# Kernel tuning notes

Measured on AMD Instinct MI355X. Metric: run time of the kernel, lower is better.

Reference implementation:

```python
import jax, jax.numpy as jnp
import numpy as np

NY, NX = 1024, 2048
DX, DT, NU, UB = 1.0, 0.1, 0.01, 1.0
NITER = 5
NLEVEL = int(np.log2(NY)) + 1  # 11
DIAG = -8.0 / (3.0 * DX * DX)  # center coefficient of the Laplacian stencil wA


def _conv(x, w, stride=1):
    # single-channel 'VALID' cross-correlation, same semantics as torch Conv2d(padding=0)
    return jax.lax.conv_general_dilated(x, w, (stride, stride), 'VALID',
                                        dimension_numbers=('NCHW', 'OIHW', 'NCHW'))


def _bc_u(u):
    # inlet (left/top/bottom) = ub, zero-gradient outflow on the right
    uu = jnp.pad(u, ((0, 0), (0, 0), (1, 1), (1, 1)))
    uu = uu.at[:, :, :, 0].set(UB)
    uu = uu.at[:, :, :, -1].set(uu[:, :, :, -2])
    uu = uu.at[:, :, 0, :].set(UB)
    uu = uu.at[:, :, -1, :].set(UB)
    return uu


def _bc_v(v):
    # v = 0 on inlet/top/bottom (zero pad), zero-gradient outflow on the right
    vv = jnp.pad(v, ((0, 0), (0, 0), (1, 1), (1, 1)))
    vv = vv.at[:, :, :, -1].set(vv[:, :, :, -2])
    return vv


def _bc_p(p):
    # zero-gradient pressure except fixed p=0 at the outlet
    pp = jnp.pad(p, ((0, 0), (0, 0), (1, 1), (1, 1)))
    pp = pp.at[:, :, :, 0].set(pp[:, :, :, 1])
    pp = pp.at[:, :, :, -1].set(0.0)
    pp = pp.at[:, :, 0, :].set(pp[:, :, 1, :])
    pp = pp.at[:, :, -1, :].set(pp[:, :, -2, :])
    return pp


def _bc_cw(a):
    # homogeneous (zero) halo for the multigrid correction
    return jnp.pad(a, ((0, 0), (0, 0), (1, 1), (1, 1)))


def _prolong(a):
    return jnp.repeat(jnp.repeat(a, 2, axis=2), 2, axis=3)


def _f_cycle_mg(uu, vv, p, w_xadv, w_yadv, w_A, w_res):
    b = -(_conv(uu, w_xadv) + _conv(vv, w_yadv)) / DT
    for _ in range(NITER):
        r = _conv(_bc_p(p), w_A) - b
        r_s = [r]
        for _i in range(1, NLEVEL):
            r = _conv(r, w_res, stride=2)
            r_s.append(r)
        a = jnp.zeros((1, 1, 1, 1), dtype=p.dtype)
        for i in reversed(range(1, NLEVEL)):
            if i == NLEVEL - 1:
                a = r_s[i] / DIAG
            else:
                a = a - _conv(_bc_cw(a), w_A) / DIAG + r_s[i] / DIAG
            a = _prolong(a)
        p = p - a
        p = p - _conv(_bc_p(p), w_A) / DIAG + b / DIAG
    return p


def _forward(u, v, p, sigma, w_xadv, w_yadv, w_diff, w_A, w_res):
    uu, vv, pp = _bc_u(u), _bc_v(v), _bc_p(p)
    Grapx_p = _conv(pp, w_xadv) * DT
    Grapy_p = _conv(pp, w_yadv) * DT
    ADx_u, ADy_u = _conv(uu, w_xadv), _conv(uu, w_yadv)
    ADx_v, ADy_v = _conv(vv, w_xadv), _conv(vv, w_yadv)
    AD2_u, AD2_v = _conv(uu, w_diff), _conv(vv, w_diff)
    # predictor half-step
    bu = u + 0.5 * (NU * AD2_u * DT - u * ADx_u * DT - v * ADy_u * DT) - Grapx_p
    bv = v + 0.5 * (NU * AD2_v * DT - u * ADx_v * DT - v * ADy_v * DT) - Grapy_p
    damp = 1.0 / (1.0 + DT * sigma)  # solid body Brinkman penalty
    bu, bv = bu * damp, bv * damp
    buu, bvv = _bc_u(bu), _bc_v(bv)
    ADx_u, ADy_u = _conv(buu, w_xadv), _conv(buu, w_yadv)
    ADx_v, ADy_v = _conv(bvv, w_xadv), _conv(bvv, w_yadv)
    AD2_u, AD2_v = _conv(buu, w_diff), _conv(bvv, w_diff)
    # corrector step
    u = u + NU * AD2_u * DT - bu * ADx_u * DT - bv * ADy_u * DT - Grapx_p
    v = v + NU * AD2_v * DT - bu * ADx_v * DT - bv * ADy_v * DT - Grapy_p
    u, v = u * damp, v * damp
    uu, vv = _bc_u(u), _bc_v(v)
    # pressure solve via multigrid F-cycle + projection
    p = _f_cycle_mg(uu, vv, p, w_xadv, w_yadv, w_A, w_res)
    pp = _bc_p(p)
    u = u - _conv(pp, w_xadv) * DT
    v = v - _conv(pp, w_yadv) * DT
    u, v = u * damp, v * damp
    return jnp.concatenate([u, v, p], axis=1)  # (1, 3, NY, NX)


def setup_inputs() -> dict:
    key = jax.random.key(0)
    k1, k2, k3 = jax.random.split(key, 3)
    shp = (1, 1, NY, NX)
    u = jax.random.normal(k1, shp, jnp.float32) * 0.1 + UB
    v = jax.random.normal(k2, shp, jnp.float32) * 0.1
    p = jax.random.normal(k3, shp, jnp.float32) * 0.1
    # bluff-body mask: 1/timescale inside the rectangle (Block.create_solid_body_2D)
    cor_x, cor_y = NX // 4, NY // 2
    size_x, size_y = NX // 32, NY // 8
    sigma = jnp.zeros(shp, jnp.float32)
    sigma = sigma.at[0, 0, cor_y - size_y:cor_y + size_y,
                     cor_x - size_x:cor_x + size_x].set(1e8)
    # finite-difference stencils from get_weights_linear_2D(dx)
    w_diff = jnp.array([[1., 1., 1.], [1., -8., 1.], [1., 1., 1.]],
                       jnp.float32).reshape(1, 1, 3, 3) / (3.0 * DX * DX)
    w_xadv = jnp.array([[-1., 0., 1.], [-4., 0., 4.], [-1., 0., 1.]],
                       jnp.float32).reshape(1, 1, 3, 3) / (12.0 * DX)
    w_yadv = jnp.array([[-1., -4., -1.], [0., 0., 0.], [1., 4., 1.]],
                       jnp.float32).reshape(1, 1, 3, 3) / (12.0 * DX)
    w_A = w_diff
    w_res = jnp.full((1, 1, 2, 2), 0.25, jnp.float32)
    return {"u": u, "v": v, "p": p, "sigma": sigma, "w_xadv": w_xadv,
            "w_yadv": w_yadv, "w_diff": w_diff, "w_A": w_A, "w_res": w_res}


def reference(u, v, p, sigma, w_xadv, w_yadv, w_diff, w_A, w_res):
    return _forward(u, v, p, sigma, w_xadv, w_yadv, w_diff, w_A, w_res)
```

## Files before the change

kernel.cpp:

```cpp
#include <hip/hip_runtime.h>
#include <cstdint>

#define GNY 1024
#define GNX 2048
#define GNPTS (GNY * GNX)

namespace {
constexpr float DT = 0.1f;
constexpr float NUc = 0.01f;
constexpr float INV_DIAG = -0.375f;
}

__device__ __forceinline__ float bc_u_at(const float* __restrict__ f, int y, int x) {
    if (y < 0 || y >= GNY || x < 0) return 1.0f;
    if (x >= GNX) x = GNX - 1;
    return f[y * GNX + x];
}
__device__ __forceinline__ float bc_v_at(const float* __restrict__ f, int y, int x) {
    if (y < 0 || y >= GNY || x < 0) return 0.0f;
    if (x >= GNX) x = GNX - 1;
    return f[y * GNX + x];
}
__device__ __forceinline__ float bc_p_at(const float* __restrict__ f, int y, int x) {
    if (x >= GNX) return 0.0f;
    if (x < 0) x = 0;
    y = min(max(y, 0), GNY - 1);
    return f[y * GNX + x];
}

__device__ __forceinline__ float conv_x3(const float m[3][3]) {
    return ((m[0][2] - m[0][0]) + 4.0f * (m[1][2] - m[1][0]) + (m[2][2] - m[2][0])) * (1.0f / 12.0f);
}
__device__ __forceinline__ float conv_y3(const float m[3][3]) {
    return ((m[2][0] - m[0][0]) + 4.0f * (m[2][1] - m[0][1]) + (m[2][2] - m[0][2])) * (1.0f / 12.0f);
}
__device__ __forceinline__ float conv_d3(const float m[3][3]) {
    return (m[0][0] + m[0][1] + m[0][2] + m[1][0] + m[1][2] + m[2][0] + m[2][1] + m[2][2]
            - 8.0f * m[1][1]) * (1.0f / 3.0f);
}

template <typename PG>
__device__ __forceinline__ float up_val(PG pget, float rval, int H, int W, int y, int x) {
    float m[3][3];
#pragma unroll
    for (int dy = 0; dy < 3; ++dy)
#pragma unroll
        for (int dx = 0; dx < 3; ++dx) {
            int yy = y + dy - 1, xx = x + dx - 1;
            m[dy][dx] = (yy >= 0 && yy < H && xx >= 0 && xx < W) ? pget(yy >> 1, xx >> 1) : 0.0f;
        }
    float conv = (m[0][0] + m[0][1] + m[0][2] + m[1][0] + m[1][2]
                  + m[2][0] + m[2][1] + m[2][2] - 8.0f * m[1][1]) * (1.0f / 3.0f);
    return m[1][1] - conv * INV_DIAG + rval * INV_DIAG;
}

__global__ __launch_bounds__(256) void k_front(
        const float* __restrict__ u, const float* __restrict__ v,
        const float* __restrict__ p, const float* __restrict__ sigma,
        float* __restrict__ u2g, float* __restrict__ v2g, float* __restrict__ bg,
        float* __restrict__ r1, float* __restrict__ r2, float* __restrict__ r3,
        float* __restrict__ r4, float* __restrict__ r5) {
    __shared__ float scrF[8442];
    float* sP    = scrF;
    float* sU    = scrF + 1482;
    float* sV    = scrF + 2964;
    float* sU2   = scrF + 1482;
    float* sV2   = scrF + 2672;
    float* sBu   = scrF + 4446;
    float* sBv   = scrF + 5778;
    float* sDamp = scrF + 7110;
    float* s0    = scrF + 4446;
    float* s1    = scrF + 5502;
    float* s2    = scrF + 5774;
    float* s3    = scrF + 5846;
    float* s4    = scrF + 5866;

    int t = threadIdx.x;
    int bx = blockIdx.x, by = blockIdx.y;
    int y0 = by * 32, x0 = bx * 32;
    bool edge = !(bx >= 1 && bx <= 62 && by >= 1 && by <= 30);
    bool rightcol = (bx == 63);

    if (!edge) {
        for (int i = t; i < 1444; i += 256) {
            int wy = i / 38, wx = i - wy * 38;
            int idx = (y0 - 3 + wy) * GNX + (x0 - 3 + wx);
            sP[wy * 39 + wx] = p[idx];
            sU[wy * 39 + wx] = u[idx];
            sV[wy * 39 + wx] = v[idx];
        }
    } else {
        for (int i = t; i < 1444; i += 256) {
            int wy = i / 38, wx = i - wy * 38;
            int gy = y0 - 3 + wy, gx = x0 - 3 + wx;
            sP[wy * 39 + wx] = bc_p_at(p, gy, gx);
            sU[wy * 39 + wx] = bc_u_at(u, gy, gx);
            sV[wy * 39 + wx] = bc_v_at(v, gy, gx);
        }
    }
    __syncthreads();

    for (int i = t; i < 1296; i += 256) {
        int ay = i / 36, ax = i - ay * 36;
        int gy = y0 - 2 + ay, gx = x0 - 2 + ax;
        float un[3][3], vn[3][3], pn[3][3];
#pragma unroll
        for (int dy = 0; dy < 3; ++dy)
#pragma unroll
            for (int dx = 0; dx < 3; ++dx) {
                int li = (ay + dy) * 39 + ax + dx;
                un[dy][dx] = sU[li]; vn[dy][dx] = sV[li]; pn[dy][dx] = sP[li];
            }
        float buv, bvv, dampv = 0.0f;
        bool valid = !edge || (gy >= 0 && gy < GNY && gx >= 0 && gx < GNX);
        if (valid) {
            dampv = 1.0f / (1.0f + DT * sigma[gy * GNX + gx]);
            float gxp = conv_x3(pn) * DT, gyp = conv_y3(pn) * DT;
            float uc = un[1][1], vc = vn[1][1];
            buv = (uc + 0.5f * (NUc * conv_d3(un) * DT - uc * conv_x3(un) * DT - vc * conv_y3(un) * DT) - gxp) * dampv;
            bvv = (vc + 0.5f * (NUc * conv_d3(vn) * DT - uc * conv_x3(vn) * DT - vc * conv_y3(vn) * DT) - gyp) * dampv;
        } else if (gy < 0 || gy >= GNY || gx < 0) {
            buv = 1.0f; bvv = 0.0f;
        } else {
            buv = 0.0f; bvv = 0.0f;
        }
        sBu[ay * 37 + ax] = buv;
        sBv[ay * 37 + ax] = bvv;
        sDamp[ay * 37 + ax] = dampv;
    }
    __syncthreads();

    float ucA[5], vcA[5];
    {
        int np = 0;
        for (int i = t; i < 1156; i += 256, ++np) {
            int cy = i / 34, cx = i - cy * 34;
            int li = (cy + 2) * 39 + cx + 2;
            ucA[np] = sU[li]; vcA[np] = sV[li];
        }
    }
    __syncthreads();
    {
        int np = 0;
        for (int i = t; i < 1156; i += 256, ++np) {
            int cy = i / 34, cx = i - cy * 34;
            int gy = y0 - 1 + cy, gx = x0 - 1 + cx;
            float u2_ = 0.0f, v2_ = 0.0f;
            bool valid = (gy >= 0 && gy < GNY && gx >= 0 && gx < GNX);
            if (valid) {
                float bun[3][3], bvn[3][3], pn[3][3];
                if (!rightcol) {
#pragma unroll
                    for (int dy = 0; dy < 3; ++dy)
#pragma unroll
                        for (int dx = 0; dx < 3; ++dx) {
                            int li = (cy + dy) * 37 + cx + dx;
                            bun[dy][dx] = sBu[li]; bvn[dy][dx] = sBv[li];
                            pn[dy][dx] = sP[(cy + dy + 1) * 39 + cx + dx + 1];
                        }
                } else {
#pragma unroll
                    for (int dy = 0; dy < 3; ++dy)
#pragma unroll
                        for (int dx = 0; dx < 3; ++dx) {
                            int yy = gy + dy - 1, xx = gx + dx - 1;
                            pn[dy][dx] = sP[(cy + dy + 1) * 39 + cx + dx + 1];
                            if (yy < 0 || yy >= GNY || xx < 0) { bun[dy][dx] = 1.0f; bvn[dy][dx] = 0.0f; }
                            else {
                                int cxx = (xx >= GNX) ? GNX - 1 : xx;
                                int li = (cy + dy) * 37 + (cxx - (x0 - 2));
                                bun[dy][dx] = sBu[li]; bvn[dy][dx] = sBv[li];
                            }
                        }
                }
                float gxp = conv_x3(pn) * DT, gyp = conv_y3(pn) * DT;
                float dampv = sDamp[(cy + 1) * 37 + cx + 1];
                float buc = bun[1][1], bvc = bvn[1][1];
                u2_ = (ucA[np] + NUc * conv_d3(bun) * DT - buc * conv_x3(bun) * DT - bvc * conv_y3(bun) * DT - gxp) * dampv;
                v2_ = (vcA[np] + NUc * conv_d3(bvn) * DT - buc * conv_x3(bvn) * DT - bvc * conv_y3(bvn) * DT - gyp) * dampv;
                if (cy >= 1 && cy <= 32 && cx >= 1 && cx <= 32) {
                    int idx = gy * GNX + gx;
                    u2g[idx] = u2_; v2g[idx] = v2_;
                }
            } else if (gy < 0 || gy >= GNY || gx < 0) {
                u2_ = 1.0f; v2_ = 0.0f;
            }
            sU2[cy * 35 + cx] = u2_;
            sV2[cy * 35 + cx] = v2_;
        }
    }
    __syncthreads();

    for (int i = t; i < 1024; i += 256) {
        int ty = i >> 5, tx = i & 31;
        int gy = y0 + ty, gx = x0 + tx;
        float un[3][3], vn[3][3], pn[3][3];
        if (!rightcol) {
#pragma unroll
            for (int dy = 0; dy < 3; ++dy)
#pragma unroll
                for (int dx = 0; dx < 3; ++dx) {
                    int li = (ty + dy) * 35 + tx + dx;
                    un[dy][dx] = sU2[li]; vn[dy][dx] = sV2[li];
                    pn[dy][dx] = sP[(ty + dy + 2) * 39 + tx + dx + 2];
                }
        } else {
#pragma unroll
            for (int dy = 0; dy < 3; ++dy)
#pragma unroll
                for (int dx = 0; dx < 3; ++dx) {
                    int yy = gy + dy - 1, xx = gx + dx - 1;
                    pn[dy][dx] = sP[(ty + dy + 2) * 39 + tx + dx + 2];
                    if (yy < 0 || yy >= GNY || xx < 0) { un[dy][dx] = 1.0f; vn[dy][dx] = 0.0f; }
                    else {
                        int cxx = (xx >= GNX) ? GNX - 1 : xx;
                        int li = (ty + dy) * 35 + (cxx - (x0 - 1));
                        un[dy][dx] = sU2[li]; vn[dy][dx] = sV2[li];
                    }
                }
        }
        float b_ = -(conv_x3(un) + conv_y3(vn)) * (1.0f / DT);
        bg[gy * GNX + gx] = b_;
        s0[ty * 33 + tx] = conv_d3(pn) - b_;
    }
    __syncthreads();

    { int qy = t >> 4, qx = t & 15;
      float vv = 0.25f * (s0[(2*qy)*33 + 2*qx] + s0[(2*qy)*33 + 2*qx + 1]
                        + s0[(2*qy+1)*33 + 2*qx] + s0[(2*qy+1)*33 + 2*qx + 1]);
      s1[qy*17 + qx] = vv;
      r1[(by*16 + qy)*1024 + bx*16 + qx] = vv; }
    __syncthreads();
    if (t < 64) { int qy = t >> 3, qx = t & 7;
      float vv = 0.25f * (s1[(2*qy)*17 + 2*qx] + s1[(2*qy)*17 + 2*qx + 1]
                        + s1[(2*qy+1)*17 + 2*qx] + s1[(2*qy+1)*17 + 2*qx + 1]);
      s2[qy*9 + qx] = vv;
      r2[(by*8 + qy)*512 + bx*8 + qx] = vv; }
    __syncthreads();
    if (t < 16) { int qy = t >> 2, qx = t & 3;
      float vv = 0.25f * (s2[(2*qy)*9 + 2*qx] + s2[(2*qy)*9 + 2*qx + 1]
                        + s2[(2*qy+1)*9 + 2*qx] + s2[(2*qy+1)*9 + 2*qx + 1]);
      s3[qy*5 + qx] = vv;
      r3[(by*4 + qy)*256 + bx*4 + qx] = vv; }
    __syncthreads();
    if (t < 4) { int qy = t >> 1, qx = t & 1;
      float vv = 0.25f * (s3[(2*qy)*5 + 2*qx] + s3[(2*qy)*5 + 2*qx + 1]
                        + s3[(2*qy+1)*5 + 2*qx] + s3[(2*qy+1)*5 + 2*qx + 1]);
      s4[qy*3 + qx] = vv;
      r4[(by*2 + qy)*128 + bx*2 + qx] = vv; }
    __syncthreads();
    if (t == 0)
        r5[by*64 + bx] = 0.25f * (s4[0] + s4[1] + s4[3] + s4[4]);
}

__global__ __launch_bounds__(256) void k_mg(
        const float* __restrict__ p_src, const float* __restrict__ b,
        const float* __restrict__ r1, const float* __restrict__ r2,
        const float* __restrict__ r3, const float* __restrict__ r4,
        const float* __restrict__ r5,
        float* __restrict__ p_dst,
        float* __restrict__ o1, float* __restrict__ o2, float* __restrict__ o3,
        float* __restrict__ o4, float* __restrict__ o5,
        const float* __restrict__ sigma, float* __restrict__ u_io,
        float* __restrict__ v_io, int last) {
    __shared__ float scr[3948];
    __shared__ float w6v[9], w5v[9], w4v[16], w3v[36], w2v[100], w1v[324];
    float* s5  = scr;
    float* s6  = scr + 2048;
    float* s7  = scr + 2560;
    float* s8  = scr + 2688;
    float* s9  = scr + 2720;
    float* s10 = scr + 2728;
    float* a9  = scr + 2730;
    float* a8  = scr + 2738;
    float* a7  = scr + 2770;
    float* sPp = scr;
    float* sPn = scr + 1332;
    float* s0  = scr + 2522;
    float* s1  = scr + 3578;
    float* s2  = scr + 3850;
    float* s3  = scr + 3922;
    float* s4  = scr + 3942;

    int t = threadIdx.x;
    int bx = blockIdx.x, by = blockIdx.y;
    int y0 = by * 32, x0 = bx * 32;

    for (int i = t; i < 2048; i += 256) s5[i] = r5[i];
    __syncthreads();
    for (int i = t; i < 512; i += 256) {
        int y = i >> 5, x = i & 31;
        s6[i] = 0.25f * (s5[(2*y)*64 + 2*x] + s5[(2*y)*64 + 2*x + 1]
                       + s5[(2*y+1)*64 + 2*x] + s5[(2*y+1)*64 + 2*x + 1]);
    }
    __syncthreads();
    if (t < 128) { int y = t >> 4, x = t & 15;
        s7[t] = 0.25f * (s6[(2*y)*32 + 2*x] + s6[(2*y)*32 + 2*x + 1]
                       + s6[(2*y+1)*32 + 2*x] + s6[(2*y+1)*32 + 2*x + 1]); }
    __syncthreads();
    if (t < 32) { int y = t >> 3, x = t & 7;
        s8[t] = 0.25f * (s7[(2*y)*16 + 2*x] + s7[(2*y)*16 + 2*x + 1]
                       + s7[(2*y+1)*16 + 2*x] + s7[(2*y+1)*16 + 2*x + 1]); }
    __syncthreads();
    if (t < 8) { int y = t >> 2, x = t & 3;
        s9[t] = 0.25f * (s8[(2*y)*8 + 2*x] + s8[(2*y)*8 + 2*x + 1]
                       + s8[(2*y+1)*8 + 2*x] + s8[(2*y+1)*8 + 2*x + 1]); }
    __syncthreads();
    if (t < 2)
        s10[t] = 0.25f * (s9[2*t] + s9[2*t + 1] + s9[4 + 2*t] + s9[4 + 2*t + 1]);
    __syncthreads();
    if (t < 8) { int y = t >> 2, x = t & 3;
        a9[t] = up_val([&](int py, int px) { return s10[py*2 + px] * INV_DIAG; },
                       s9[t], 2, 4, y, x); }
    __syncthreads();
    if (t < 32) { int y = t >> 3, x = t & 7;
        a8[t] = up_val([&](int py, int px) { return a9[py*4 + px]; },
                       s8[t], 4, 8, y, x); }
    __syncthreads();
    if (t < 128) { int y = t >> 4, x = t & 15;
        a7[t] = up_val([&](int py, int px) { return a8[py*8 + px]; },
                       s7[t], 8, 16, y, x); }
    __syncthreads();

    int w6ylo = (by - 2) >> 1, w6xlo = (bx - 2) >> 1;
    int w5ylo = by - 1,        w5xlo = bx - 1;
    int w4ylo = 2*by - 1,      w4xlo = 2*bx - 1;
    int w3ylo = 4*by - 1,      w3xlo = 4*bx - 1;
    int w2ylo = 8*by - 1,      w2xlo = 8*bx - 1;
    int w1ylo = 16*by - 1,     w1xlo = 16*bx - 1;

    if (t < 9) { int gy = w6ylo + t/3, gx = w6xlo + t%3;
        w6v[t] = (gy >= 0 && gy < 16 && gx >= 0 && gx < 32)
            ? up_val([&](int py, int px) { return a7[py*16 + px]; },
                     s6[gy*32 + gx], 16, 32, gy, gx) : 0.0f; }
    __syncthreads();
    if (t < 9) { int gy = w5ylo + t/3, gx = w5xlo + t%3;
        w5v[t] = (gy >= 0 && gy < 32 && gx >= 0 && gx < 64)
            ? up_val([&](int py, int px) { return w6v[(py - w6ylo)*3 + (px - w6xlo)]; },
                     s5[gy*64 + gx], 32, 64, gy, gx) : 0.0f; }
    __syncthreads();
    if (t < 16) { int gy = w4ylo + t/4, gx = w4xlo + t%4;
        w4v[t] = (gy >= 0 && gy < 64 && gx >= 0 && gx < 128)
            ? up_val([&](int py, int px) { return w5v[(py - w5ylo)*3 + (px - w5xlo)]; },
                     r4[gy*128 + gx], 64, 128, gy, gx) : 0.0f; }
    __syncthreads();
    if (t < 36) { int gy = w3ylo + t/6, gx = w3xlo + t%6;
        w3v[t] = (gy >= 0 && gy < 128 && gx >= 0 && gx < 256)
            ? up_val([&](int py, int px) { return w4v[(py - w4ylo)*4 + (px - w4xlo)]; },
                     r3[gy*256 + gx], 128, 256, gy, gx) : 0.0f; }
    __syncthreads();
    if (t < 100) { int gy = w2ylo + t/10, gx = w2xlo + t%10;
        w2v[t] = (gy >= 0 && gy < 256 && gx >= 0 && gx < 512)
            ? up_val([&](int py, int px) { return w3v[(py - w3ylo)*6 + (px - w3xlo)]; },
                     r2[gy*512 + gx], 256, 512, gy, gx) : 0.0f; }
    __syncthreads();
    for (int i = t; i < 324; i += 256) { int gy = w1ylo + i/18, gx = w1xlo + i%18;
        w1v[i] = (gy >= 0 && gy < 512 && gx >= 0 && gx < 1024)
            ? up_val([&](int py, int px) { return w2v[(py - w2ylo)*10 + (px - w2xlo)]; },
                     r1[gy*1024 + gx], 512, 1024, gy, gx) : 0.0f; }
    __syncthreads();

    for (int i = t; i < 1296; i += 256) {
        int wy = i / 36, wx = i - wy * 36;
        int yy = y0 - 2 + wy, xx = x0 - 2 + wx;
        float v = 0.0f;
        if (xx < GNX) {
            int cy = min(max(yy, 0), GNY - 1);
            int cx = xx < 0 ? 0 : xx;
            v = p_src[cy*GNX + cx] - w1v[((cy >> 1) - w1ylo)*18 + ((cx >> 1) - w1xlo)];
        }
        sPp[wy*37 + wx] = v;
    }
    __syncthreads();
    for (int i = t; i < 1156; i += 256) {
        int wy = i / 34, wx = i - wy * 34;
        int yy = y0 - 1 + wy, xx = x0 - 1 + wx;
        float v = 0.0f;
        if (xx < GNX) {
            int cy = min(max(yy, 0), GNY - 1);
            int cx = xx < 0 ? 0 : xx;
            int rb = cy - y0 + 2, cb = cx - x0 + 2;
            float m[3][3];
#pragma unroll
            for (int dy = 0; dy < 3; ++dy)
#pragma unroll
                for (int dx = 0; dx < 3; ++dx)
                    m[dy][dx] = sPp[(rb + dy - 1)*37 + (cb + dx - 1)];
            float conv = (m[0][0] + m[0][1] + m[0][2] + m[1][0] + m[1][2]
                          + m[2][0] + m[2][1] + m[2][2] - 8.0f*m[1][1]) * (1.0f / 3.0f);
            v = m[1][1] - conv * INV_DIAG + b[cy*GNX + cx] * INV_DIAG;
        }
        sPn[wy*35 + wx] = v;
    }
    __syncthreads();
    for (int i = t; i < 1024; i += 256) {
        int ty = i >> 5, tx = i & 31;
        p_dst[(y0 + ty)*GNX + x0 + tx] = sPn[(ty + 1)*35 + (tx + 1)];
    }

    if (!last) {
        for (int i = t; i < 1024; i += 256) {
            int ty = i >> 5, tx = i & 31;
            float m[3][3];
#pragma unroll
            for (int dy = 0; dy < 3; ++dy)
#pragma unroll
                for (int dx = 0; dx < 3; ++dx)
                    m[dy][dx] = sPn[(ty + dy)*35 + (tx + dx)];
            s0[ty*33 + tx] = conv_d3(m) - b[(y0 + ty)*GNX + x0 + tx];
        }
        __syncthreads();
        { int qy = t >> 4, qx = t & 15;
          float v = 0.25f * (s0[(2*qy)*33 + 2*qx] + s0[(2*qy)*33 + 2*qx + 1]
                           + s0[(2*qy+1)*33 + 2*qx] + s0[(2*qy+1)*33 + 2*qx + 1]);
          s1[qy*17 + qx] = v;
          o1[(by*16 + qy)*1024 + bx*16 + qx] = v; }
        __syncthreads();
        if (t < 64) { int qy = t >> 3, qx = t & 7;
          float v = 0.25f * (s1[(2*qy)*17 + 2*qx] + s1[(2*qy)*17 + 2*qx + 1]
                           + s1[(2*qy+1)*17 + 2*qx] + s1[(2*qy+1)*17 + 2*qx + 1]);
          s2[qy*9 + qx] = v;
          o2[(by*8 + qy)*512 + bx*8 + qx] = v; }
        __syncthreads();
        if (t < 16) { int qy = t >> 2, qx = t & 3;
          float v = 0.25f * (s2[(2*qy)*9 + 2*qx] + s2[(2*qy)*9 + 2*qx + 1]
                           + s2[(2*qy+1)*9 + 2*qx] + s2[(2*qy+1)*9 + 2*qx + 1]);
          s3[qy*5 + qx] = v;
          o3[(by*4 + qy)*256 + bx*4 + qx] = v; }
        __syncthreads();
        if (t < 4) { int qy = t >> 1, qx = t & 1;
          float v = 0.25f * (s3[(2*qy)*5 + 2*qx] + s3[(2*qy)*5 + 2*qx + 1]
                           + s3[(2*qy+1)*5 + 2*qx] + s3[(2*qy+1)*5 + 2*qx + 1]);
          s4[qy*3 + qx] = v;
          o4[(by*2 + qy)*128 + bx*2 + qx] = v; }
        __syncthreads();
        if (t == 0)
            o5[by*64 + bx] = 0.25f * (s4[0] + s4[1] + s4[3] + s4[4]);
    } else {
        for (int i = t; i < 1024; i += 256) {
            int ty = i >> 5, tx = i & 31;
            float m[3][3];
#pragma unroll
            for (int dy = 0; dy < 3; ++dy)
#pragma unroll
                for (int dx = 0; dx < 3; ++dx)
                    m[dy][dx] = sPn[(ty + dy)*35 + (tx + dx)];
            int idx = (y0 + ty)*GNX + x0 + tx;
            float damp = 1.0f / (1.0f + DT * sigma[idx]);
            u_io[idx] = (u_io[idx] - conv_x3(m) * DT) * damp;
            v_io[idx] = (v_io[idx] - conv_y3(m) * DT) * damp;
        }
    }
}

extern "C" void kernel_launch(void* const* d_in, const int* in_sizes, int n_in,
                              void* d_out, int out_size, void* d_ws, size_t ws_size,
                              hipStream_t stream) {
    (void)in_sizes; (void)n_in; (void)out_size; (void)ws_size;
    const float* u_in  = (const float*)d_in[0];
    const float* v_in  = (const float*)d_in[1];
    const float* p_in  = (const float*)d_in[2];
    const float* sigma = (const float*)d_in[3];

    float* out_u = (float*)d_out;
    float* out_v = out_u + GNPTS;
    float* out_p = out_u + 2 * (size_t)GNPTS;

    float* ws   = (float*)d_ws;
    float* b    = ws;
    float* p_ws = b + (size_t)GNPTS;
    float* base = p_ws + (size_t)GNPTS;
    float* A_[5], * B_[5];
    size_t lsz[5] = {524288, 131072, 32768, 8192, 2048};
    float* cur = base;
    for (int l = 0; l < 5; ++l) { A_[l] = cur; cur += lsz[l]; }
    for (int l = 0; l < 5; ++l) { B_[l] = cur; cur += lsz[l]; }

    dim3 grdT(GNX / 32, GNY / 32), blkT(256);

    k_front<<<grdT, blkT, 0, stream>>>(u_in, v_in, p_in, sigma,
                                       out_u, out_v, b,
                                       A_[0], A_[1], A_[2], A_[3], A_[4]);

    const float* p_cur = p_in;
    float* p_bufs[2] = { out_p, p_ws };
    for (int it = 0; it < 5; ++it) {
        float** rp = (it % 2 == 0) ? A_ : B_;
        float** wp = (it % 2 == 0) ? B_ : A_;
        float* p_next = p_bufs[it % 2];
        int last = (it == 4) ? 1 : 0;
        k_mg<<<grdT, blkT, 0, stream>>>(p_cur, b,
                                        rp[0], rp[1], rp[2], rp[3], rp[4],
                                        p_next,
                                        wp[0], wp[1], wp[2], wp[3], wp[4],
                                        sigma, out_u, out_v, last);
        p_cur = p_next;
    }
}
```

Baseline: 220.1 us.

## Prefetch multigrid inputs into shared memory before the serial coarse-grid chain

In the multigrid kernel, the fine-grid pressure window, the b window and the per-block r1–r4 patches are now loaded into one larger shared buffer at kernel start, together with r5. Their global-memory latency can then overlap instead of sitting behind the serial chain of tiny coarse-level restrict and prolong steps. Later stages, including the residual subtraction of b, read these shared copies rather than global memory. In the first kernel, the damping factor from sigma is computed during the initial load phase instead of inside the stencil loop. The cost is roughly 25KB of shared memory per block, which may lower occupancy, and the boundary-halo stencil now indexes unclamped window positions, which could change edge values.

```diff
diff --git a/kernel.cpp b/kernel.cpp
--- a/kernel.cpp
+++ b/kernel.cpp
@@ -89,6 +89,10 @@
             sU[wy * 39 + wx] = u[idx];
             sV[wy * 39 + wx] = v[idx];
         }
+        for (int i = t; i < 1296; i += 256) {
+            int ay = i / 36, ax = i - ay * 36;
+            sDamp[ay * 37 + ax] = 1.0f / (1.0f + DT * sigma[(y0 - 2 + ay) * GNX + x0 - 2 + ax]);
+        }
     } else {
         for (int i = t; i < 1444; i += 256) {
             int wy = i / 38, wx = i - wy * 38;
@@ -97,6 +101,14 @@
             sU[wy * 39 + wx] = bc_u_at(u, gy, gx);
             sV[wy * 39 + wx] = bc_v_at(v, gy, gx);
         }
+        for (int i = t; i < 1296; i += 256) {
+            int ay = i / 36, ax = i - ay * 36;
+            int gy = y0 - 2 + ay, gx = x0 - 2 + ax;
+            float d = 0.0f;
+            if (gy >= 0 && gy < GNY && gx >= 0 && gx < GNX)
+                d = 1.0f / (1.0f + DT * sigma[gy * GNX + gx]);
+            sDamp[ay * 37 + ax] = d;
+        }
     }
     __syncthreads();
 
@@ -111,10 +123,10 @@
                 int li = (ay + dy) * 39 + ax + dx;
                 un[dy][dx] = sU[li]; vn[dy][dx] = sV[li]; pn[dy][dx] = sP[li];
             }
-        float buv, bvv, dampv = 0.0f;
+        float buv, bvv;
         bool valid = !edge || (gy >= 0 && gy < GNY && gx >= 0 && gx < GNX);
         if (valid) {
-            dampv = 1.0f / (1.0f + DT * sigma[gy * GNX + gx]);
+            float dampv = sDamp[ay * 37 + ax];
             float gxp = conv_x3(pn) * DT, gyp = conv_y3(pn) * DT;
             float uc = un[1][1], vc = vn[1][1];
             buv = (uc + 0.5f * (NUc * conv_d3(un) * DT - uc * conv_x3(un) * DT - vc * conv_y3(un) * DT) - gxp) * dampv;
@@ -126,7 +138,6 @@
         }
         sBu[ay * 37 + ax] = buv;
         sBv[ay * 37 + ax] = bvv;
-        sDamp[ay * 37 + ax] = dampv;
     }
     __syncthreads();
 
@@ -263,64 +274,39 @@
         float* __restrict__ o4, float* __restrict__ o5,
         const float* __restrict__ sigma, float* __restrict__ u_io,
         float* __restrict__ v_io, int last) {
-    __shared__ float scr[3948];
-    __shared__ float w6v[9], w5v[9], w4v[16], w3v[36], w2v[100], w1v[324];
-    float* s5  = scr;
-    float* s6  = scr + 2048;
-    float* s7  = scr + 2560;
-    float* s8  = scr + 2688;
-    float* s9  = scr + 2720;
-    float* s10 = scr + 2728;
-    float* a9  = scr + 2730;
-    float* a8  = scr + 2738;
-    float* a7  = scr + 2770;
-    float* sPp = scr;
-    float* sPn = scr + 1332;
-    float* s0  = scr + 2522;
-    float* s1  = scr + 3578;
-    float* s2  = scr + 3850;
-    float* s3  = scr + 3922;
-    float* s4  = scr + 3942;
+    __shared__ float L[6390];
+    float* gR5 = L;
+    float* gP  = L + 2048;
+    float* gB  = L + 3380;
+    float* gR1 = L + 4570;
+    float* gR2 = L + 4894;
+    float* gR3 = L + 4994;
+    float* gR4 = L + 5030;
+    float* s6  = L + 5046;
+    float* s7  = L + 5558;
+    float* s8  = L + 5686;
+    float* s9  = L + 5718;
+    float* s10 = L + 5726;
+    float* a9  = L + 5728;
+    float* a8  = L + 5736;
+    float* a7  = L + 5768;
+    float* w6v = L + 5896;
+    float* w5v = L + 5905;
+    float* w4v = L + 5914;
+    float* w3v = L + 5930;
+    float* w2v = L + 5966;
+    float* w1v = L + 6066;
+    float* sPp = L;
+    float* sPn = L + 2048;
+    float* s0  = L;
+    float* s1  = L + 1056;
+    float* s2  = L + 1328;
+    float* s3  = L + 1400;
+    float* s4  = L + 1420;
 
     int t = threadIdx.x;
     int bx = blockIdx.x, by = blockIdx.y;
     int y0 = by * 32, x0 = bx * 32;
-
-    for (int i = t; i < 2048; i += 256) s5[i] = r5[i];
-    __syncthreads();
-    for (int i = t; i < 512; i += 256) {
-        int y = i >> 5, x = i & 31;
-        s6[i] = 0.25f * (s5[(2*y)*64 + 2*x] + s5[(2*y)*64 + 2*x + 1]
-                       + s5[(2*y+1)*64 + 2*x] + s5[(2*y+1)*64 + 2*x + 1]);
-    }
-    __syncthreads();
-    if (t < 128) { int y = t >> 4, x = t & 15;
-        s7[t] = 0.25f * (s6[(2*y)*32 + 2*x] + s6[(2*y)*32 + 2*x + 1]
-                       + s6[(2*y+1)*32 + 2*x] + s6[(2*y+1)*32 + 2*x + 1]); }
-    __syncthreads();
-    if (t < 32) { int y = t >> 3, x = t & 7;
-        s8[t] = 0.25f * (s7[(2*y)*16 + 2*x] + s7[(2*y)*16 + 2*x + 1]
-                       + s7[(2*y+1)*16 + 2*x] + s7[(2*y+1)*16 + 2*x + 1]); }
-    __syncthreads();
-    if (t < 8) { int y = t >> 2, x = t & 3;
-        s9[t] = 0.25f * (s8[(2*y)*8 + 2*x] + s8[(2*y)*8 + 2*x + 1]
-                       + s8[(2*y+1)*8 + 2*x] + s8[(2*y+1)*8 + 2*x + 1]); }
-    __syncthreads();
-    if (t < 2)
-        s10[t] = 0.25f * (s9[2*t] + s9[2*t + 1] + s9[4 + 2*t] + s9[4 + 2*t + 1]);
-    __syncthreads();
-    if (t < 8) { int y = t >> 2, x = t & 3;
-        a9[t] = up_val([&](int py, int px) { return s10[py*2 + px] * INV_DIAG; },
-                       s9[t], 2, 4, y, x); }
-    __syncthreads();
-    if (t < 32) { int y = t >> 3, x = t & 7;
-        a8[t] = up_val([&](int py, int px) { return a9[py*4 + px]; },
-                       s8[t], 4, 8, y, x); }
-    __syncthreads();
-    if (t < 128) { int y = t >> 4, x = t & 15;
-        a7[t] = up_val([&](int py, int px) { return a8[py*8 + px]; },
-                       s7[t], 8, 16, y, x); }
-    __syncthreads();
 
     int w6ylo = (by - 2) >> 1, w6xlo = (bx - 2) >> 1;
     int w5ylo = by - 1,        w5xlo = bx - 1;
@@ -329,66 +315,129 @@
     int w2ylo = 8*by - 1,      w2xlo = 8*bx - 1;
     int w1ylo = 16*by - 1,     w1xlo = 16*bx - 1;
 
-    if (t < 9) { int gy = w6ylo + t/3, gx = w6xlo + t%3;
-        w6v[t] = (gy >= 0 && gy < 16 && gx >= 0 && gx < 32)
-            ? up_val([&](int py, int px) { return a7[py*16 + px]; },
-                     s6[gy*32 + gx], 16, 32, gy, gx) : 0.0f; }
-    __syncthreads();
-    if (t < 9) { int gy = w5ylo + t/3, gx = w5xlo + t%3;
-        w5v[t] = (gy >= 0 && gy < 32 && gx >= 0 && gx < 64)
-            ? up_val([&](int py, int px) { return w6v[(py - w6ylo)*3 + (px - w6xlo)]; },
-                     s5[gy*64 + gx], 32, 64, gy, gx) : 0.0f; }
-    __syncthreads();
-    if (t < 16) { int gy = w4ylo + t/4, gx = w4xlo + t%4;
-        w4v[t] = (gy >= 0 && gy < 64 && gx >= 0 && gx < 128)
-            ? up_val([&](int py, int px) { return w5v[(py - w5ylo)*3 + (px - w5xlo)]; },
-                     r4[gy*128 + gx], 64, 128, gy, gx) : 0.0f; }
-    __syncthreads();
-    if (t < 36) { int gy = w3ylo + t/6, gx = w3xlo + t%6;
-        w3v[t] = (gy >= 0 && gy < 128 && gx >= 0 && gx < 256)
-            ? up_val([&](int py, int px) { return w4v[(py - w4ylo)*4 + (px - w4xlo)]; },
-                     r3[gy*256 + gx], 128, 256, gy, gx) : 0.0f; }
-    __syncthreads();
-    if (t < 100) { int gy = w2ylo + t/10, gx = w2xlo + t%10;
-        w2v[t] = (gy >= 0 && gy < 256 && gx >= 0 && gx < 512)
-            ? up_val([&](int py, int px) { return w3v[(py - w3ylo)*6 + (px - w3xlo)]; },
-                     r2[gy*512 + gx], 256, 512, gy, gx) : 0.0f; }
-    __syncthreads();
-    for (int i = t; i < 324; i += 256) { int gy = w1ylo + i/18, gx = w1xlo + i%18;
-        w1v[i] = (gy >= 0 && gy < 512 && gx >= 0 && gx < 1024)
-            ? up_val([&](int py, int px) { return w2v[(py - w2ylo)*10 + (px - w2xlo)]; },
-                     r1[gy*1024 + gx], 512, 1024, gy, gx) : 0.0f; }
-    __syncthreads();
-
+    for (int i = t; i < 2048; i += 256) gR5[i] = r5[i];
     for (int i = t; i < 1296; i += 256) {
         int wy = i / 36, wx = i - wy * 36;
         int yy = y0 - 2 + wy, xx = x0 - 2 + wx;
         float v = 0.0f;
         if (xx < GNX) {
-            int cy = min(max(yy, 0), GNY - 1);
-            int cx = xx < 0 ? 0 : xx;
-            v = p_src[cy*GNX + cx] - w1v[((cy >> 1) - w1ylo)*18 + ((cx >> 1) - w1xlo)];
-        }
-        sPp[wy*37 + wx] = v;
-    }
-    __syncthreads();
+            int cy = min(max(yy, 0), GNY - 1), cx = xx < 0 ? 0 : xx;
+            v = p_src[cy * GNX + cx];
+        }
+        gP[wy * 37 + wx] = v;
+    }
     for (int i = t; i < 1156; i += 256) {
         int wy = i / 34, wx = i - wy * 34;
         int yy = y0 - 1 + wy, xx = x0 - 1 + wx;
         float v = 0.0f;
         if (xx < GNX) {
-            int cy = min(max(yy, 0), GNY - 1);
-            int cx = xx < 0 ? 0 : xx;
-            int rb = cy - y0 + 2, cb = cx - x0 + 2;
+            int cy = min(max(yy, 0), GNY - 1), cx = xx < 0 ? 0 : xx;
+            v = b[cy * GNX + cx];
+        }
+        gB[wy * 35 + wx] = v;
+    }
+    for (int i = t; i < 324; i += 256) {
+        int gy = w1ylo + i / 18, gx = w1xlo + i % 18;
+        gR1[i] = (gy >= 0 && gy < 512 && gx >= 0 && gx < 1024) ? r1[gy * 1024 + gx] : 0.0f;
+    }
+    if (t < 100) { int gy = w2ylo + t / 10, gx = w2xlo + t % 10;
+        gR2[t] = (gy >= 0 && gy < 256 && gx >= 0 && gx < 512) ? r2[gy * 512 + gx] : 0.0f; }
+    if (t < 36)  { int gy = w3ylo + t / 6, gx = w3xlo + t % 6;
+        gR3[t] = (gy >= 0 && gy < 128 && gx >= 0 && gx < 256) ? r3[gy * 256 + gx] : 0.0f; }
+    if (t < 16)  { int gy = w4ylo + t / 4, gx = w4xlo + t % 4;
+        gR4[t] = (gy >= 0 && gy < 64 && gx >= 0 && gx < 128) ? r4[gy * 128 + gx] : 0.0f; }
+    __syncthreads();
+
+    for (int i = t; i < 512; i += 256) {
+        int y = i >> 5, x = i & 31;
+        s6[i] = 0.25f * (gR5[(2*y)*64 + 2*x] + gR5[(2*y)*64 + 2*x + 1]
+                       + gR5[(2*y+1)*64 + 2*x] + gR5[(2*y+1)*64 + 2*x + 1]);
+    }
+    __syncthreads();
+    if (t < 128) { int y = t >> 4, x = t & 15;
+        s7[t] = 0.25f * (s6[(2*y)*32 + 2*x] + s6[(2*y)*32 + 2*x + 1]
+                       + s6[(2*y+1)*32 + 2*x] + s6[(2*y+1)*32 + 2*x + 1]); }
+    __syncthreads();
+    if (t < 32) { int y = t >> 3, x = t & 7;
+        s8[t] = 0.25f * (s7[(2*y)*16 + 2*x] + s7[(2*y)*16 + 2*x + 1]
+                       + s7[(2*y+1)*16 + 2*x] + s7[(2*y+1)*16 + 2*x + 1]); }
+    __syncthreads();
+    if (t < 8) { int y = t >> 2, x = t & 3;
+        s9[t] = 0.25f * (s8[(2*y)*8 + 2*x] + s8[(2*y)*8 + 2*x + 1]
+                       + s8[(2*y+1)*8 + 2*x] + s8[(2*y+1)*8 + 2*x + 1]); }
+    __syncthreads();
+    if (t < 2)
+        s10[t] = 0.25f * (s9[2*t] + s9[2*t + 1] + s9[4 + 2*t] + s9[4 + 2*t + 1]);
+    __syncthreads();
+    if (t < 8) { int y = t >> 2, x = t & 3;
+        a9[t] = up_val([&](int py, int px) { return s10[py*2 + px] * INV_DIAG; },
+                       s9[t], 2, 4, y, x); }
+    __syncthreads();
+    if (t < 32) { int y = t >> 3, x = t & 7;
+        a8[t] = up_val([&](int py, int px) { return a9[py*4 + px]; },
+                       s8[t], 4, 8, y, x); }
+    __syncthreads();
+    if (t < 128) { int y = t >> 4, x = t & 15;
+        a7[t] = up_val([&](int py, int px) { return a8[py*8 + px]; },
+                       s7[t], 8, 16, y, x); }
+    __syncthreads();
+
+    if (t < 9) { int gy = w6ylo + t/3, gx = w6xlo + t%3;
+        w6v[t] = (gy >= 0 && gy < 16 && gx >= 0 && gx < 32)
+            ? up_val([&](int py, int px) { return a7[py*16 + px]; },
+                     s6[gy*32 + gx], 16, 32, gy, gx) : 0.0f; }
+    __syncthreads();
+    if (t < 9) { int gy = w5ylo + t/3, gx = w5xlo + t%3;
+        w5v[t] = (gy >= 0 && gy < 32 && gx >= 0 && gx < 64)
+            ? up_val([&](int py, int px) { return w6v[(py - w6ylo)*3 + (px - w6xlo)]; },
+                     gR5[gy*64 + gx], 32, 64, gy, gx) : 0.0f; }
+    __syncthreads();
+    if (t < 16) { int gy = w4ylo + t/4, gx = w4xlo + t%4;
+        w4v[t] = (gy >= 0 && gy < 64 && gx >= 0 && gx < 128)
+            ? up_val([&](int py, int px) { return w5v[(py - w5ylo)*3 + (px - w5xlo)]; },
+                     gR4[t], 64, 128, gy, gx) : 0.0f; }
+    __syncthreads();
+    if (t < 36) { int gy = w3ylo + t/6, gx = w3xlo + t%6;
+        w3v[t] = (gy >= 0 && gy < 128 && gx >= 0 && gx < 256)
+            ? up_val([&](int py, int px) { return w4v[(py - w4ylo)*4 + (px - w4xlo)]; },
+                     gR3[t], 128, 256, gy, gx) : 0.0f; }
+    __syncthreads();
+    if (t < 100) { int gy = w2ylo + t/10, gx = w2xlo + t%10;
+        w2v[t] = (gy >= 0 && gy < 256 && gx >= 0 && gx < 512)
+            ? up_val([&](int py, int px) { return w3v[(py - w3ylo)*6 + (px - w3xlo)]; },
+                     gR2[t], 256, 512, gy, gx) : 0.0f; }
+    __syncthreads();
+    for (int i = t; i < 324; i += 256) { int gy = w1ylo + i/18, gx = w1xlo + i%18;
+        w1v[i] = (gy >= 0 && gy < 512 && gx >= 0 && gx < 1024)
+            ? up_val([&](int py, int px) { return w2v[(py - w2ylo)*10 + (px - w2xlo)]; },
+                     gR1[i], 512, 1024, gy, gx) : 0.0f; }
+    __syncthreads();
+
+    for (int i = t; i < 1296; i += 256) {
+        int wy = i / 36, wx = i - wy * 36;
+        int yy = y0 - 2 + wy, xx = x0 - 2 + wx;
+        float v = 0.0f;
+        if (xx < GNX) {
+            int cy = min(max(yy, 0), GNY - 1), cx = xx < 0 ? 0 : xx;
+            v = gP[wy*37 + wx] - w1v[((cy >> 1) - w1ylo)*18 + ((cx >> 1) - w1xlo)];
+        }
+        sPp[wy*37 + wx] = v;
+    }
+    __syncthreads();
+    for (int i = t; i < 1156; i += 256) {
+        int wy = i / 34, wx = i - wy * 34;
+        int xx = x0 - 1 + wx;
+        float v = 0.0f;
+        if (xx < GNX) {
             float m[3][3];
 #pragma unroll
             for (int dy = 0; dy < 3; ++dy)
 #pragma unroll
                 for (int dx = 0; dx < 3; ++dx)
-                    m[dy][dx] = sPp[(rb + dy - 1)*37 + (cb + dx - 1)];
+                    m[dy][dx] = sPp[(wy + dy)*37 + (wx + dx)];
             float conv = (m[0][0] + m[0][1] + m[0][2] + m[1][0] + m[1][2]
                           + m[2][0] + m[2][1] + m[2][2] - 8.0f*m[1][1]) * (1.0f / 3.0f);
-            v = m[1][1] - conv * INV_DIAG + b[cy*GNX + cx] * INV_DIAG;
+            v = m[1][1] - conv * INV_DIAG + gB[wy*35 + wx] * INV_DIAG;
         }
         sPn[wy*35 + wx] = v;
     }
@@ -407,7 +456,7 @@
 #pragma unroll
                 for (int dx = 0; dx < 3; ++dx)
                     m[dy][dx] = sPn[(ty + dy)*35 + (tx + dx)];
-            s0[ty*33 + tx] = conv_d3(m) - b[(y0 + ty)*GNX + x0 + tx];
+            s0[ty*33 + tx] = conv_d3(m) - gB[(ty + 1)*35 + (tx + 1)];
         }
         __syncthreads();
         { int qy = t >> 4, qx = t & 15;
```

Result: slower. 291.6 us (+32.5%).
